# Kernel optimization log

Measured on AMD Instinct MI355X. Metric: run time of the kernel, lower is better.

The kernel has to match this reference:

```python
import jax, jax.numpy as jnp
import numpy as np

B, N = 1, 1024
C_S, C_Z, N_HEAD, C_HEAD = 384, 128, 16, 24
HC = N_HEAD * C_HEAD


def _ln(x, eps=1e-5):
    m = jnp.mean(x, axis=-1, keepdims=True)
    v = jnp.var(x, axis=-1, keepdims=True)
    return (x - m) / jnp.sqrt(v + eps)


def setup_inputs() -> dict:
    key = jax.random.key(0)
    ks = jax.random.split(key, 24)
    w = lambda k, shp: (jax.random.normal(k, shp, jnp.float32) * 0.02)
    return {
        "a_i": jax.random.normal(ks[0], (B, N, C_S), jnp.float32),
        "s_i": jax.random.normal(ks[1], (B, N, C_S), jnp.float32),
        "z_ij": jax.random.normal(ks[2], (B, N, N, C_Z), jnp.float32),
        # AdaLN params
        "adaln_lns_w": jnp.ones((C_S,), jnp.float32),      # layer_norm_s weight (no bias)
        "adaln_ws": w(ks[3], (C_S, C_S)),                   # linear_s weight
        "adaln_bs": jnp.zeros((C_S,), jnp.float32),         # linear_s bias
        "adaln_wns": w(ks[4], (C_S, C_S)),                  # linear_no_bias_s
        # attention projections
        "wq": w(ks[5], (C_S, HC)),
        "bq": jnp.zeros((HC,), jnp.float32),
        "wk": w(ks[6], (C_S, HC)),
        "wv": w(ks[7], (C_S, HC)),
        # pair bias
        "lnb_w": jnp.ones((C_Z,), jnp.float32),
        "lnb_b": jnp.zeros((C_Z,), jnp.float32),
        "wb": w(ks[8], (C_Z, N_HEAD)),
        # gate + output
        "wg": w(ks[9], (C_S, HC)),
        "wo": w(ks[10], (HC, C_S)),
        # final conditioning gate (bias init -2.0 per module)
        "ws": w(ks[11], (C_S, C_S)),
        "bs": jnp.full((C_S,), -2.0, jnp.float32),
    }


def reference(a_i, s_i, z_ij, adaln_lns_w, adaln_ws, adaln_bs, adaln_wns,
              wq, bq, wk, wv, lnb_w, lnb_b, wb, wg, wo, ws, bs):
    b, n, _ = a_i.shape
    H, D = N_HEAD, C_HEAD
    # AdaLN: a <- sigmoid(Lin(s)) * LN(a) + Lin_nb(s)
    a = _ln(a_i)
    s = _ln(s_i) * adaln_lns_w
    a = jax.nn.sigmoid(s @ adaln_ws + adaln_bs) * a + s @ adaln_wns
    # QKV projections -> [b, i, h, d]
    q = (a @ wq + bq).reshape(b, n, H, D)
    k = (a @ wk).reshape(b, n, H, D)
    v = (a @ wv).reshape(b, n, H, D)
    # pair bias [b, h, i, j]
    bias = jnp.einsum('bijc,ch->bhij', _ln(z_ij) * lnb_w + lnb_b, wb)
    # gate [b, i, h, d]
    g = jax.nn.sigmoid(a @ wg).reshape(b, n, H, D)
    logits = jnp.einsum('bihd,bjhd->bhij', q, k) / jnp.sqrt(jnp.float32(D)) + bias
    A = jax.nn.softmax(logits, axis=-1)
    o = jnp.einsum('bhij,bjhd->bihd', A, v) * g
    o = o.reshape(b, n, H * D) @ wo
    # final gate uses raw s_i
    return jax.nn.sigmoid(s_i @ ws + bs) * o
```

## Files before the change

### kernel.cpp

```cpp
#include <hip/hip_runtime.h>
#include <hip/hip_bf16.h>
#include <math.h>

#define N_SEQ 1024
#define CS 384
#define CZ 128
#define NH 16
#define CH 24

typedef float  floatx4 __attribute__((ext_vector_type(4)));
typedef short  shortx8 __attribute__((ext_vector_type(8)));
typedef unsigned int uintx4 __attribute__((ext_vector_type(4)));

__device__ __forceinline__ unsigned short f2bf(float f){
  union { float fv; unsigned u; } c; c.fv = f;
  unsigned u = c.u;
  return (unsigned short)((u + 0x7fffu + ((u >> 16) & 1u)) >> 16);
}
__device__ __forceinline__ float bf2f(unsigned short s){
  union { unsigned u; float fv; } c; c.u = ((unsigned)s) << 16; return c.fv;
}
__device__ __forceinline__ float bf_lo(unsigned u){
  union { unsigned uu; float f; } c; c.uu = u << 16; return c.f;
}
__device__ __forceinline__ float bf_hi(unsigned u){
  union { unsigned uu; float f; } c; c.uu = u & 0xffff0000u; return c.f;
}
__device__ __forceinline__ float sigmoidf_(float x){ return 1.f / (1.f + __expf(-x)); }

__global__ __launch_bounds__(128) void ln_kernel(
    const float* __restrict__ a_i, const float* __restrict__ s_i,
    const float* __restrict__ lns_w,
    float* __restrict__ a_ln, float* __restrict__ s_ln)
{
  int i = blockIdx.x;
  int t = threadIdx.x;
  float av[3], sv[3];
  float sa = 0.f, qa = 0.f, ss = 0.f, qs = 0.f;
  #pragma unroll
  for (int e = 0; e < 3; ++e){
    int c = t + 128*e;
    float a = a_i[(size_t)i*CS + c];
    float s = s_i[(size_t)i*CS + c];
    av[e] = a; sv[e] = s;
    sa += a; qa += a*a; ss += s; qs += s*s;
  }
  #pragma unroll
  for (int off = 1; off < 64; off <<= 1){
    sa += __shfl_xor(sa, off);
    qa += __shfl_xor(qa, off);
    ss += __shfl_xor(ss, off);
    qs += __shfl_xor(qs, off);
  }
  __shared__ float red[2][4];
  if ((t & 63) == 0){
    int w = t >> 6;
    red[w][0] = sa; red[w][1] = qa; red[w][2] = ss; red[w][3] = qs;
  }
  __syncthreads();
  const float inv = 1.f / CS;
  float Sa = red[0][0] + red[1][0];
  float Qa = red[0][1] + red[1][1];
  float Ss = red[0][2] + red[1][2];
  float Qs = red[0][3] + red[1][3];
  float ma = Sa*inv, va = Qa*inv - ma*ma, ra = rsqrtf(va + 1e-5f);
  float ms = Ss*inv, vs = Qs*inv - ms*ms, rs = rsqrtf(vs + 1e-5f);
  #pragma unroll
  for (int e = 0; e < 3; ++e){
    int c = t + 128*e;
    a_ln[(size_t)i*CS + c] = (av[e] - ma) * ra;
    s_ln[(size_t)i*CS + c] = (sv[e] - ms) * rs * lns_w[c];
  }
}

__global__ __launch_bounds__(384) void gemm_kernel(
    const float* __restrict__ X, const float* __restrict__ W1,
    const float* __restrict__ B1, const float* __restrict__ W2,
    const float* __restrict__ extra,
    float* __restrict__ OUT1, float* __restrict__ OUT2, int mode)
{
  int r0 = blockIdx.x * 4;
  int t  = threadIdx.x;
  int ct = t % 96;
  int rg = t / 96;
  int c0 = ct * 4;
  __shared__ float xl[4][CS];
  #pragma unroll
  for (int rr = 0; rr < 4; ++rr)
    xl[rr][t] = X[(size_t)(r0+rr)*CS + t];
  __syncthreads();
  float acc1[4] = {0.f,0.f,0.f,0.f};
  float acc2[4] = {0.f,0.f,0.f,0.f};
  if (mode <= 2){
    for (int k = 0; k < CS; k += 4){
      floatx4 s4 = *(const floatx4*)&xl[rg][k];
      #pragma unroll
      for (int kk = 0; kk < 4; ++kk){
        floatx4 w1 = *(const floatx4*)&W1[(size_t)(k+kk)*CS + c0];
        floatx4 w2 = *(const floatx4*)&W2[(size_t)(k+kk)*CS + c0];
        #pragma unroll
        for (int cc = 0; cc < 4; ++cc){
          acc1[cc] += s4[kk] * w1[cc];
          acc2[cc] += s4[kk] * w2[cc];
        }
      }
    }
  } else {
    for (int k = 0; k < CS; k += 4){
      floatx4 s4 = *(const floatx4*)&xl[rg][k];
      #pragma unroll
      for (int kk = 0; kk < 4; ++kk){
        floatx4 w1 = *(const floatx4*)&W1[(size_t)(k+kk)*CS + c0];
        #pragma unroll
        for (int cc = 0; cc < 4; ++cc)
          acc1[cc] += s4[kk] * w1[cc];
      }
    }
  }
  int r = r0 + rg;
  size_t ob = (size_t)r * CS + c0;
  if (mode == 0){
    #pragma unroll
    for (int cc = 0; cc < 4; ++cc)
      OUT1[ob+cc] = sigmoidf_(acc1[cc] + B1[c0+cc]) * extra[ob+cc] + acc2[cc];
  } else if (mode == 1){
    #pragma unroll
    for (int cc = 0; cc < 4; ++cc){
      OUT1[ob+cc] = acc1[cc] + B1[c0+cc];
      OUT2[ob+cc] = acc2[cc];
    }
  } else if (mode == 2){
    #pragma unroll
    for (int cc = 0; cc < 4; ++cc){
      OUT1[ob+cc] = acc1[cc];
      OUT2[ob+cc] = sigmoidf_(acc2[cc]);
    }
  } else if (mode == 3){
    #pragma unroll
    for (int cc = 0; cc < 4; ++cc)
      OUT1[ob+cc] = acc1[cc];
  } else {
    #pragma unroll
    for (int cc = 0; cc < 4; ++cc)
      OUT1[ob+cc] = sigmoidf_(acc1[cc] + B1[c0+cc]) * extra[ob+cc];
  }
}

__global__ __launch_bounds__(256) void bias_kernel(
    const float* __restrict__ z, const float* __restrict__ lnb_w,
    const float* __restrict__ lnb_b, const float* __restrict__ wb,
    unsigned short* __restrict__ bias)
{
  int i    = blockIdx.x >> 4;
  int j0   = (blockIdx.x & 15) * 64;
  int wave = threadIdx.x >> 6;
  int lane = threadIdx.x & 63;
  int m    = lane & 15;
  int q    = lane >> 4;
  int jbase = j0 + wave * 16;

  shortx8 bfrag[4];
  float sumw = 0.f, sumb = 0.f;
  #pragma unroll
  for (int s = 0; s < 4; ++s){
    #pragma unroll
    for (int jj = 0; jj < 8; ++jj){
      int c = q*8 + jj + 32*s;
      float lw = lnb_w[c];
      float lb = lnb_b[c];
      float w  = wb[c*NH + m];
      bfrag[s][jj] = (short)f2bf(lw * w);
      sumw += lw * w;
      sumb += lb * w;
    }
  }
  sumw += __shfl_xor(sumw, 16); sumw += __shfl_xor(sumw, 32);
  sumb += __shfl_xor(sumb, 16); sumb += __shfl_xor(sumb, 32);

  const float* zrow = z + ((size_t)i * N_SEQ + (size_t)(jbase + m)) * CZ;
  floatx4 acc = {0.f, 0.f, 0.f, 0.f};
  float sum = 0.f, sq = 0.f;
  #pragma unroll
  for (int s = 0; s < 4; ++s){
    floatx4 z0 = *(const floatx4*)(zrow + q*8 + 32*s);
    floatx4 z1 = *(const floatx4*)(zrow + q*8 + 32*s + 4);
    shortx8 af;
    #pragma unroll
    for (int e = 0; e < 4; ++e){
      sum += z0[e]; sq += z0[e]*z0[e];
      sum += z1[e]; sq += z1[e]*z1[e];
      af[e]   = (short)f2bf(z0[e]);
      af[e+4] = (short)f2bf(z1[e]);
    }
    acc = __builtin_amdgcn_mfma_f32_16x16x32_bf16(af, bfrag[s], acc, 0, 0, 0);
  }
  sum += __shfl_xor(sum, 16); sum += __shfl_xor(sum, 32);
  sq  += __shfl_xor(sq , 16); sq  += __shfl_xor(sq , 32);
  float mean = sum * (1.f/CZ);
  float var  = sq  * (1.f/CZ) - mean*mean;
  float rstd = rsqrtf(var + 1e-5f);

  __shared__ float ob[NH][65];
  #pragma unroll
  for (int r = 0; r < 4; ++r){
    int row = q*4 + r;
    float mr = __shfl(mean, row);
    float rr = __shfl(rstd, row);
    ob[m][wave*16 + row] = rr * (acc[r] - mr * sumw) + sumb;
  }
  __syncthreads();
  size_t base = (size_t)i * N_SEQ + j0;
  #pragma unroll
  for (int rep = 0; rep < 4; ++rep){
    int idx = threadIdx.x + rep*256;
    int hh = idx >> 6;
    int jj = idx & 63;
    bias[(size_t)hh * ((size_t)N_SEQ*N_SEQ) + base + jj] = f2bf(ob[hh][jj]);
  }
}

#define TJ 128
#define KROW 20
__global__ __launch_bounds__(256) void attn_kernel(
    const float* __restrict__ qq, const float* __restrict__ kk,
    const float* __restrict__ vv, const float* __restrict__ gg,
    const unsigned short* __restrict__ bias, float* __restrict__ att)
{
  int h  = blockIdx.x & 15;
  int i0 = (blockIdx.x >> 4) * 16;
  int il = threadIdx.x & 15;
  int jg = threadIdx.x >> 4;

  __shared__ unsigned int smem[TJ*KROW*2];

  float qr[24];
  {
    const float* qs = qq + (size_t)(i0+il)*CS + h*CH;
    #pragma unroll
    for (int e = 0; e < 6; ++e){
      floatx4 t4 = *(const floatx4*)(qs + 4*e);
      qr[4*e] = t4[0]; qr[4*e+1] = t4[1]; qr[4*e+2] = t4[2]; qr[4*e+3] = t4[3];
    }
  }
  const float scale = 0.20412414523193154f;
  float lrun = 0.f;
  float o[24];
  #pragma unroll
  for (int d = 0; d < 24; ++d) o[d] = 0.f;

  for (int jt = 0; jt < 8; ++jt){
    __syncthreads();
    {
      int row  = threadIdx.x >> 1;
      int half = threadIdx.x & 1;
      const float* ks = kk + (size_t)(jt*TJ + row)*CS + h*CH + half*12;
      const float* vs = vv + (size_t)(jt*TJ + row)*CS + h*CH + half*12;
      unsigned int* kd = smem + row*KROW + half*6;
      unsigned int* vd = smem + TJ*KROW + row*KROW + half*6;
      #pragma unroll
      for (int e = 0; e < 6; ++e){
        kd[e] = (unsigned)f2bf(ks[2*e]) | ((unsigned)f2bf(ks[2*e+1]) << 16);
        vd[e] = (unsigned)f2bf(vs[2*e]) | ((unsigned)f2bf(vs[2*e+1]) << 16);
      }
    }
    __syncthreads();
    const unsigned short* bptr = bias + (size_t)h*((size_t)N_SEQ*N_SEQ)
                               + (size_t)(i0+il)*N_SEQ + jt*TJ;
    #pragma unroll
    for (int tt = 0; tt < 8; ++tt){
      int jl = jg + 16*tt;
      uintx4 k0 = *(const uintx4*)&smem[jl*KROW];
      uintx4 k1 = *(const uintx4*)&smem[jl*KROW + 4];
      uintx4 k2 = *(const uintx4*)&smem[jl*KROW + 8];
      float dot = 0.f;
      #pragma unroll
      for (int e = 0; e < 4; ++e){
        dot += bf_lo(k0[e])*qr[2*e]      + bf_hi(k0[e])*qr[2*e+1];
        dot += bf_lo(k1[e])*qr[8+2*e]    + bf_hi(k1[e])*qr[8+2*e+1];
        dot += bf_lo(k2[e])*qr[16+2*e]   + bf_hi(k2[e])*qr[16+2*e+1];
      }
      float p = __expf(dot * scale + bf2f(bptr[jl]));
      lrun += p;
      uintx4 v0 = *(const uintx4*)&smem[TJ*KROW + jl*KROW];
      uintx4 v1 = *(const uintx4*)&smem[TJ*KROW + jl*KROW + 4];
      uintx4 v2 = *(const uintx4*)&smem[TJ*KROW + jl*KROW + 8];
      #pragma unroll
      for (int e = 0; e < 4; ++e){
        o[2*e]      += p * bf_lo(v0[e]);  o[2*e+1]    += p * bf_hi(v0[e]);
        o[8+2*e]    += p * bf_lo(v1[e]);  o[8+2*e+1]  += p * bf_hi(v1[e]);
        o[16+2*e]   += p * bf_lo(v2[e]);  o[16+2*e+1] += p * bf_hi(v2[e]);
      }
    }
  }
  __syncthreads();
  #pragma unroll
  for (int d = 0; d < 24; ++d){
    o[d] += __shfl_xor(o[d], 16);
    o[d] += __shfl_xor(o[d], 32);
  }
  lrun += __shfl_xor(lrun, 16);
  lrun += __shfl_xor(lrun, 32);
  float* mgf = (float*)smem;
  int lane = threadIdx.x & 63;
  int w    = threadIdx.x >> 6;
  if (lane < 16){
    float* slot = mgf + (w*16 + lane)*25;
    slot[0] = lrun;
    #pragma unroll
    for (int d = 0; d < 24; ++d) slot[1+d] = o[d];
  }
  __syncthreads();
  if (threadIdx.x < 16){
    int ii = threadIdx.x;
    float L = 0.f, O[24];
    #pragma unroll
    for (int d = 0; d < 24; ++d) O[d] = 0.f;
    for (int w2 = 0; w2 < 4; ++w2){
      const float* slot = mgf + (w2*16 + ii)*25;
      L += slot[0];
      #pragma unroll
      for (int d = 0; d < 24; ++d) O[d] += slot[1+d];
    }
    const float* gs = gg + (size_t)(i0+ii)*CS + h*CH;
    float* os = att + (size_t)(i0+ii)*CS + h*CH;
    float invL = 1.f / L;
    #pragma unroll
    for (int d = 0; d < 24; ++d) os[d] = O[d] * invL * gs[d];
  }
}

extern "C" void kernel_launch(void* const* d_in, const int* in_sizes, int n_in,
                              void* d_out, int out_size, void* d_ws, size_t ws_size,
                              hipStream_t stream) {
  const float* a_i     = (const float*)d_in[0];
  const float* s_i     = (const float*)d_in[1];
  const float* z_ij    = (const float*)d_in[2];
  const float* lns_w   = (const float*)d_in[3];
  const float* ada_ws  = (const float*)d_in[4];
  const float* ada_bs  = (const float*)d_in[5];
  const float* ada_wns = (const float*)d_in[6];
  const float* wq      = (const float*)d_in[7];
  const float* bq      = (const float*)d_in[8];
  const float* wk      = (const float*)d_in[9];
  const float* wv      = (const float*)d_in[10];
  const float* lnb_w   = (const float*)d_in[11];
  const float* lnb_b   = (const float*)d_in[12];
  const float* wb      = (const float*)d_in[13];
  const float* wg      = (const float*)d_in[14];
  const float* wo      = (const float*)d_in[15];
  const float* wsm     = (const float*)d_in[16];
  const float* bsv     = (const float*)d_in[17];

  const size_t RC = (size_t)N_SEQ * CS;
  float* wsf  = (float*)d_ws;
  float* s_ln = wsf;
  float* a_ln = wsf + RC;
  float* a    = wsf + 2*RC;
  float* qv   = wsf + 3*RC;
  float* kv   = wsf + 4*RC;
  float* vvp  = wsf + 5*RC;
  float* gv   = wsf + 6*RC;
  float* attb = wsf + 7*RC;
  float* tmp  = wsf + 8*RC;
  unsigned short* biasw = (unsigned short*)(wsf + 9*RC);

  ln_kernel<<<N_SEQ, 128, 0, stream>>>(a_i, s_i, lns_w, a_ln, s_ln);
  gemm_kernel<<<N_SEQ/4, 384, 0, stream>>>(s_ln, ada_ws, ada_bs, ada_wns, a_ln, a, nullptr, 0);
  gemm_kernel<<<N_SEQ/4, 384, 0, stream>>>(a, wq, bq, wk, nullptr, qv, kv, 1);
  gemm_kernel<<<N_SEQ/4, 384, 0, stream>>>(a, wv, nullptr, wg, nullptr, vvp, gv, 2);
  bias_kernel<<<N_SEQ*16, 256, 0, stream>>>(z_ij, lnb_w, lnb_b, wb, biasw);
  attn_kernel<<<N_SEQ, 256, 0, stream>>>(qv, kv, vvp, gv, biasw, attb);
  gemm_kernel<<<N_SEQ/4, 384, 0, stream>>>(attb, wo, nullptr, nullptr, nullptr, tmp, nullptr, 3);
  gemm_kernel<<<N_SEQ/4, 384, 0, stream>>>(s_i, wsm, bsv, nullptr, tmp, (float*)d_out, nullptr, 4);
}
```

Measured before the change: 1.169 ms.

## Fuse LayerNorm into AdaLN GEMM, merge QKVG and output GEMMs, precompute bias weights

Folds the row LayerNorms into the AdaLN projection kernel and merges the Q/K/V/G projections into one kernel. The two output GEMMs (wo and the s_i gate) become a single kernel, so the intermediate buffers and several launches go away. The folded LayerNorm-times-wb weights and their sums are computed once in a tiny prep kernel rather than in every bias block. The K/V staging in attention now uses vectorized loads and stores. Higher register pressure in the merged GEMM kernels could reduce occupancy.

```diff
diff --git a/kernel.cpp b/kernel.cpp
--- a/kernel.cpp
+++ b/kernel.cpp
@@ -11,6 +11,7 @@
 typedef float  floatx4 __attribute__((ext_vector_type(4)));
 typedef short  shortx8 __attribute__((ext_vector_type(8)));
 typedef unsigned int uintx4 __attribute__((ext_vector_type(4)));
+typedef unsigned int uintx2 __attribute__((ext_vector_type(2)));
 
 __device__ __forceinline__ unsigned short f2bf(float f){
   union { float fv; unsigned u; } c; c.fv = f;
@@ -28,127 +29,213 @@
 }
 __device__ __forceinline__ float sigmoidf_(float x){ return 1.f / (1.f + __expf(-x)); }
 
-__global__ __launch_bounds__(128) void ln_kernel(
+__global__ __launch_bounds__(256) void prep_kernel(
+    const float* __restrict__ lnb_w, const float* __restrict__ lnb_b,
+    const float* __restrict__ wb,
+    unsigned short* __restrict__ wprodT, float* __restrict__ sums)
+{
+  int t = threadIdx.x;
+  int h = t >> 4;
+  int g = t & 15;
+  float pw = 0.f, pb = 0.f;
+  unsigned short loc[8];
+  #pragma unroll
+  for (int e = 0; e < 8; ++e){
+    int c = g*8 + e;
+    float lw = lnb_w[c], lb = lnb_b[c], w = wb[c*NH + h];
+    float p = lw * w;
+    loc[e] = f2bf(p);
+    pw += p; pb += lb * w;
+  }
+  #pragma unroll
+  for (int e = 0; e < 8; ++e) wprodT[h*CZ + g*8 + e] = loc[e];
+  #pragma unroll
+  for (int off = 1; off < 16; off <<= 1){
+    pw += __shfl_xor(pw, off);
+    pb += __shfl_xor(pb, off);
+  }
+  if (g == 0){ sums[h] = pw; sums[16+h] = pb; }
+}
+
+__global__ __launch_bounds__(384) void adaln_kernel(
     const float* __restrict__ a_i, const float* __restrict__ s_i,
     const float* __restrict__ lns_w,
-    float* __restrict__ a_ln, float* __restrict__ s_ln)
-{
-  int i = blockIdx.x;
-  int t = threadIdx.x;
-  float av[3], sv[3];
-  float sa = 0.f, qa = 0.f, ss = 0.f, qs = 0.f;
-  #pragma unroll
-  for (int e = 0; e < 3; ++e){
-    int c = t + 128*e;
-    float a = a_i[(size_t)i*CS + c];
-    float s = s_i[(size_t)i*CS + c];
-    av[e] = a; sv[e] = s;
-    sa += a; qa += a*a; ss += s; qs += s*s;
-  }
-  #pragma unroll
-  for (int off = 1; off < 64; off <<= 1){
-    sa += __shfl_xor(sa, off);
-    qa += __shfl_xor(qa, off);
-    ss += __shfl_xor(ss, off);
-    qs += __shfl_xor(qs, off);
-  }
-  __shared__ float red[2][4];
-  if ((t & 63) == 0){
-    int w = t >> 6;
-    red[w][0] = sa; red[w][1] = qa; red[w][2] = ss; red[w][3] = qs;
-  }
-  __syncthreads();
-  const float inv = 1.f / CS;
-  float Sa = red[0][0] + red[1][0];
-  float Qa = red[0][1] + red[1][1];
-  float Ss = red[0][2] + red[1][2];
-  float Qs = red[0][3] + red[1][3];
-  float ma = Sa*inv, va = Qa*inv - ma*ma, ra = rsqrtf(va + 1e-5f);
-  float ms = Ss*inv, vs = Qs*inv - ms*ms, rs = rsqrtf(vs + 1e-5f);
-  #pragma unroll
-  for (int e = 0; e < 3; ++e){
-    int c = t + 128*e;
-    a_ln[(size_t)i*CS + c] = (av[e] - ma) * ra;
-    s_ln[(size_t)i*CS + c] = (sv[e] - ms) * rs * lns_w[c];
-  }
-}
-
-__global__ __launch_bounds__(384) void gemm_kernel(
-    const float* __restrict__ X, const float* __restrict__ W1,
-    const float* __restrict__ B1, const float* __restrict__ W2,
-    const float* __restrict__ extra,
-    float* __restrict__ OUT1, float* __restrict__ OUT2, int mode)
+    const float* __restrict__ W1, const float* __restrict__ B1,
+    const float* __restrict__ W2, float* __restrict__ OUT)
 {
   int r0 = blockIdx.x * 4;
   int t  = threadIdx.x;
-  int ct = t % 96;
-  int rg = t / 96;
-  int c0 = ct * 4;
-  __shared__ float xl[4][CS];
-  #pragma unroll
-  for (int rr = 0; rr < 4; ++rr)
-    xl[rr][t] = X[(size_t)(r0+rr)*CS + t];
-  __syncthreads();
+  __shared__ float xs[4][CS];
+  __shared__ float xa[4][CS];
+  __shared__ float red[6][16];
+  float av[4], sv[4], pa[4], qa[4], ps[4], qs[4];
+  #pragma unroll
+  for (int rr = 0; rr < 4; ++rr){
+    float a = a_i[(size_t)(r0+rr)*CS + t];
+    float s = s_i[(size_t)(r0+rr)*CS + t];
+    av[rr] = a; sv[rr] = s;
+    pa[rr] = a; qa[rr] = a*a; ps[rr] = s; qs[rr] = s*s;
+  }
+  #pragma unroll
+  for (int off = 1; off < 64; off <<= 1){
+    #pragma unroll
+    for (int rr = 0; rr < 4; ++rr){
+      pa[rr] += __shfl_xor(pa[rr], off);
+      qa[rr] += __shfl_xor(qa[rr], off);
+      ps[rr] += __shfl_xor(ps[rr], off);
+      qs[rr] += __shfl_xor(qs[rr], off);
+    }
+  }
+  int w = t >> 6;
+  if ((t & 63) == 0){
+    #pragma unroll
+    for (int rr = 0; rr < 4; ++rr){
+      red[w][rr] = pa[rr]; red[w][4+rr] = qa[rr];
+      red[w][8+rr] = ps[rr]; red[w][12+rr] = qs[rr];
+    }
+  }
+  __syncthreads();
+  float lw = lns_w[t];
+  const float inv = 1.f / CS;
+  #pragma unroll
+  for (int rr = 0; rr < 4; ++rr){
+    float Sa=0.f, Qa=0.f, Ss=0.f, Qs=0.f;
+    #pragma unroll
+    for (int w2 = 0; w2 < 6; ++w2){
+      Sa += red[w2][rr]; Qa += red[w2][4+rr];
+      Ss += red[w2][8+rr]; Qs += red[w2][12+rr];
+    }
+    float ma = Sa*inv, va = Qa*inv - ma*ma, ra = rsqrtf(va + 1e-5f);
+    float ms = Ss*inv, vs = Qs*inv - ms*ms, rs = rsqrtf(vs + 1e-5f);
+    xa[rr][t] = (av[rr] - ma) * ra;
+    xs[rr][t] = (sv[rr] - ms) * rs * lw;
+  }
+  __syncthreads();
+  int ct = t % 96, rg = t / 96, c0 = ct * 4;
   float acc1[4] = {0.f,0.f,0.f,0.f};
   float acc2[4] = {0.f,0.f,0.f,0.f};
-  if (mode <= 2){
-    for (int k = 0; k < CS; k += 4){
-      floatx4 s4 = *(const floatx4*)&xl[rg][k];
-      #pragma unroll
-      for (int kk = 0; kk < 4; ++kk){
-        floatx4 w1 = *(const floatx4*)&W1[(size_t)(k+kk)*CS + c0];
-        floatx4 w2 = *(const floatx4*)&W2[(size_t)(k+kk)*CS + c0];
-        #pragma unroll
-        for (int cc = 0; cc < 4; ++cc){
-          acc1[cc] += s4[kk] * w1[cc];
-          acc2[cc] += s4[kk] * w2[cc];
-        }
+  #pragma unroll 2
+  for (int k = 0; k < CS; k += 4){
+    floatx4 s4 = *(const floatx4*)&xs[rg][k];
+    floatx4 w1[4], w2[4];
+    #pragma unroll
+    for (int j = 0; j < 4; ++j){
+      size_t o = (size_t)(k+j)*CS + c0;
+      w1[j] = *(const floatx4*)&W1[o];
+      w2[j] = *(const floatx4*)&W2[o];
+    }
+    #pragma unroll
+    for (int j = 0; j < 4; ++j)
+      #pragma unroll
+      for (int cc = 0; cc < 4; ++cc){
+        acc1[cc] += s4[j] * w1[j][cc];
+        acc2[cc] += s4[j] * w2[j][cc];
       }
-    }
-  } else {
-    for (int k = 0; k < CS; k += 4){
-      floatx4 s4 = *(const floatx4*)&xl[rg][k];
-      #pragma unroll
-      for (int kk = 0; kk < 4; ++kk){
-        floatx4 w1 = *(const floatx4*)&W1[(size_t)(k+kk)*CS + c0];
-        #pragma unroll
-        for (int cc = 0; cc < 4; ++cc)
-          acc1[cc] += s4[kk] * w1[cc];
-      }
-    }
   }
   int r = r0 + rg;
   size_t ob = (size_t)r * CS + c0;
-  if (mode == 0){
-    #pragma unroll
-    for (int cc = 0; cc < 4; ++cc)
-      OUT1[ob+cc] = sigmoidf_(acc1[cc] + B1[c0+cc]) * extra[ob+cc] + acc2[cc];
-  } else if (mode == 1){
-    #pragma unroll
-    for (int cc = 0; cc < 4; ++cc){
-      OUT1[ob+cc] = acc1[cc] + B1[c0+cc];
-      OUT2[ob+cc] = acc2[cc];
-    }
-  } else if (mode == 2){
-    #pragma unroll
-    for (int cc = 0; cc < 4; ++cc){
-      OUT1[ob+cc] = acc1[cc];
-      OUT2[ob+cc] = sigmoidf_(acc2[cc]);
-    }
-  } else if (mode == 3){
-    #pragma unroll
-    for (int cc = 0; cc < 4; ++cc)
-      OUT1[ob+cc] = acc1[cc];
-  } else {
-    #pragma unroll
-    for (int cc = 0; cc < 4; ++cc)
-      OUT1[ob+cc] = sigmoidf_(acc1[cc] + B1[c0+cc]) * extra[ob+cc];
-  }
+  #pragma unroll
+  for (int cc = 0; cc < 4; ++cc)
+    OUT[ob+cc] = sigmoidf_(acc1[cc] + B1[c0+cc]) * xa[rg][c0+cc] + acc2[cc];
+}
+
+__global__ __launch_bounds__(384) void qkvg_kernel(
+    const float* __restrict__ A, const float* __restrict__ wq,
+    const float* __restrict__ bq, const float* __restrict__ wk,
+    const float* __restrict__ wv, const float* __restrict__ wg,
+    float* __restrict__ qv, float* __restrict__ kv,
+    float* __restrict__ vv, float* __restrict__ gv)
+{
+  int r0 = blockIdx.x * 4;
+  int t  = threadIdx.x;
+  __shared__ float xl[4][CS];
+  #pragma unroll
+  for (int rr = 0; rr < 4; ++rr)
+    xl[rr][t] = A[(size_t)(r0+rr)*CS + t];
+  __syncthreads();
+  int ct = t % 96, rg = t / 96, c0 = ct * 4;
+  float aq[4]={0.f,0.f,0.f,0.f}, ak[4]={0.f,0.f,0.f,0.f};
+  float av4[4]={0.f,0.f,0.f,0.f}, ag[4]={0.f,0.f,0.f,0.f};
+  #pragma unroll 2
+  for (int k = 0; k < CS; k += 4){
+    floatx4 x4 = *(const floatx4*)&xl[rg][k];
+    floatx4 q[4], kk4[4], v4[4], g4[4];
+    #pragma unroll
+    for (int j = 0; j < 4; ++j){
+      size_t o = (size_t)(k+j)*CS + c0;
+      q[j]   = *(const floatx4*)&wq[o];
+      kk4[j] = *(const floatx4*)&wk[o];
+      v4[j]  = *(const floatx4*)&wv[o];
+      g4[j]  = *(const floatx4*)&wg[o];
+    }
+    #pragma unroll
+    for (int j = 0; j < 4; ++j)
+      #pragma unroll
+      for (int cc = 0; cc < 4; ++cc){
+        aq[cc]  += x4[j] * q[j][cc];
+        ak[cc]  += x4[j] * kk4[j][cc];
+        av4[cc] += x4[j] * v4[j][cc];
+        ag[cc]  += x4[j] * g4[j][cc];
+      }
+  }
+  int r = r0 + rg;
+  size_t ob = (size_t)r * CS + c0;
+  #pragma unroll
+  for (int cc = 0; cc < 4; ++cc){
+    qv[ob+cc] = aq[cc] + bq[c0+cc];
+    kv[ob+cc] = ak[cc];
+    vv[ob+cc] = av4[cc];
+    gv[ob+cc] = sigmoidf_(ag[cc]);
+  }
+}
+
+__global__ __launch_bounds__(384) void final_kernel(
+    const float* __restrict__ att, const float* __restrict__ wo,
+    const float* __restrict__ s_i, const float* __restrict__ wsm,
+    const float* __restrict__ bsv, float* __restrict__ OUT)
+{
+  int r0 = blockIdx.x * 4;
+  int t  = threadIdx.x;
+  __shared__ float xo[4][CS];
+  __shared__ float xsI[4][CS];
+  #pragma unroll
+  for (int rr = 0; rr < 4; ++rr){
+    xo[rr][t]  = att[(size_t)(r0+rr)*CS + t];
+    xsI[rr][t] = s_i[(size_t)(r0+rr)*CS + t];
+  }
+  __syncthreads();
+  int ct = t % 96, rg = t / 96, c0 = ct * 4;
+  float acc1[4] = {0.f,0.f,0.f,0.f};
+  float acc2[4] = {0.f,0.f,0.f,0.f};
+  #pragma unroll 2
+  for (int k = 0; k < CS; k += 4){
+    floatx4 o4 = *(const floatx4*)&xo[rg][k];
+    floatx4 s4 = *(const floatx4*)&xsI[rg][k];
+    floatx4 w1[4], w2[4];
+    #pragma unroll
+    for (int j = 0; j < 4; ++j){
+      size_t o = (size_t)(k+j)*CS + c0;
+      w1[j] = *(const floatx4*)&wo[o];
+      w2[j] = *(const floatx4*)&wsm[o];
+    }
+    #pragma unroll
+    for (int j = 0; j < 4; ++j)
+      #pragma unroll
+      for (int cc = 0; cc < 4; ++cc){
+        acc1[cc] += o4[j] * w1[j][cc];
+        acc2[cc] += s4[j] * w2[j][cc];
+      }
+  }
+  int r = r0 + rg;
+  size_t ob = (size_t)r * CS + c0;
+  #pragma unroll
+  for (int cc = 0; cc < 4; ++cc)
+    OUT[ob+cc] = sigmoidf_(acc2[cc] + bsv[c0+cc]) * acc1[cc];
 }
 
 __global__ __launch_bounds__(256) void bias_kernel(
-    const float* __restrict__ z, const float* __restrict__ lnb_w,
-    const float* __restrict__ lnb_b, const float* __restrict__ wb,
+    const float* __restrict__ z,
+    const unsigned short* __restrict__ wprodT, const float* __restrict__ sums,
     unsigned short* __restrict__ bias)
 {
   int i    = blockIdx.x >> 4;
@@ -159,23 +246,13 @@
   int q    = lane >> 4;
   int jbase = j0 + wave * 16;
 
+  const unsigned short* wp = wprodT + m*CZ;
   shortx8 bfrag[4];
-  float sumw = 0.f, sumb = 0.f;
-  #pragma unroll
-  for (int s = 0; s < 4; ++s){
-    #pragma unroll
-    for (int jj = 0; jj < 8; ++jj){
-      int c = q*8 + jj + 32*s;
-      float lw = lnb_w[c];
-      float lb = lnb_b[c];
-      float w  = wb[c*NH + m];
-      bfrag[s][jj] = (short)f2bf(lw * w);
-      sumw += lw * w;
-      sumb += lb * w;
-    }
-  }
-  sumw += __shfl_xor(sumw, 16); sumw += __shfl_xor(sumw, 32);
-  sumb += __shfl_xor(sumb, 16); sumb += __shfl_xor(sumb, 32);
+  #pragma unroll
+  for (int s = 0; s < 4; ++s)
+    bfrag[s] = *(const shortx8*)(wp + q*8 + 32*s);
+  float sumw = sums[m];
+  float sumb = sums[16+m];
 
   const float* zrow = z + ((size_t)i * N_SEQ + (size_t)(jbase + m)) * CZ;
   floatx4 acc = {0.f, 0.f, 0.f, 0.f};
@@ -255,13 +332,33 @@
       int half = threadIdx.x & 1;
       const float* ks = kk + (size_t)(jt*TJ + row)*CS + h*CH + half*12;
       const float* vs = vv + (size_t)(jt*TJ + row)*CS + h*CH + half*12;
+      floatx4 ka = *(const floatx4*)(ks);
+      floatx4 kb = *(const floatx4*)(ks+4);
+      floatx4 kc = *(const floatx4*)(ks+8);
+      floatx4 va = *(const floatx4*)(vs);
+      floatx4 vb = *(const floatx4*)(vs+4);
+      floatx4 vc = *(const floatx4*)(vs+8);
       unsigned int* kd = smem + row*KROW + half*6;
       unsigned int* vd = smem + TJ*KROW + row*KROW + half*6;
-      #pragma unroll
-      for (int e = 0; e < 6; ++e){
-        kd[e] = (unsigned)f2bf(ks[2*e]) | ((unsigned)f2bf(ks[2*e+1]) << 16);
-        vd[e] = (unsigned)f2bf(vs[2*e]) | ((unsigned)f2bf(vs[2*e+1]) << 16);
-      }
+      uintx2 p0, p1, p2;
+      p0[0] = (unsigned)f2bf(ka[0]) | ((unsigned)f2bf(ka[1])<<16);
+      p0[1] = (unsigned)f2bf(ka[2]) | ((unsigned)f2bf(ka[3])<<16);
+      p1[0] = (unsigned)f2bf(kb[0]) | ((unsigned)f2bf(kb[1])<<16);
+      p1[1] = (unsigned)f2bf(kb[2]) | ((unsigned)f2bf(kb[3])<<16);
+      p2[0] = (unsigned)f2bf(kc[0]) | ((unsigned)f2bf(kc[1])<<16);
+      p2[1] = (unsigned)f2bf(kc[2]) | ((unsigned)f2bf(kc[3])<<16);
+      *(uintx2*)(kd)   = p0;
+      *(uintx2*)(kd+2) = p1;
+      *(uintx2*)(kd+4) = p2;
+      p0[0] = (unsigned)f2bf(va[0]) | ((unsigned)f2bf(va[1])<<16);
+      p0[1] = (unsigned)f2bf(va[2]) | ((unsigned)f2bf(va[3])<<16);
+      p1[0] = (unsigned)f2bf(vb[0]) | ((unsigned)f2bf(vb[1])<<16);
+      p1[1] = (unsigned)f2bf(vb[2]) | ((unsigned)f2bf(vb[3])<<16);
+      p2[0] = (unsigned)f2bf(vc[0]) | ((unsigned)f2bf(vc[1])<<16);
+      p2[1] = (unsigned)f2bf(vc[2]) | ((unsigned)f2bf(vc[3])<<16);
+      *(uintx2*)(vd)   = p0;
+      *(uintx2*)(vd+2) = p1;
+      *(uintx2*)(vd+4) = p2;
     }
     __syncthreads();
     const unsigned short* bptr = bias + (size_t)h*((size_t)N_SEQ*N_SEQ)
@@ -353,23 +450,20 @@
 
   const size_t RC = (size_t)N_SEQ * CS;
   float* wsf  = (float*)d_ws;
-  float* s_ln = wsf;
-  float* a_ln = wsf + RC;
-  float* a    = wsf + 2*RC;
-  float* qv   = wsf + 3*RC;
-  float* kv   = wsf + 4*RC;
-  float* vvp  = wsf + 5*RC;
-  float* gv   = wsf + 6*RC;
-  float* attb = wsf + 7*RC;
-  float* tmp  = wsf + 8*RC;
-  unsigned short* biasw = (unsigned short*)(wsf + 9*RC);
-
-  ln_kernel<<<N_SEQ, 128, 0, stream>>>(a_i, s_i, lns_w, a_ln, s_ln);
-  gemm_kernel<<<N_SEQ/4, 384, 0, stream>>>(s_ln, ada_ws, ada_bs, ada_wns, a_ln, a, nullptr, 0);
-  gemm_kernel<<<N_SEQ/4, 384, 0, stream>>>(a, wq, bq, wk, nullptr, qv, kv, 1);
-  gemm_kernel<<<N_SEQ/4, 384, 0, stream>>>(a, wv, nullptr, wg, nullptr, vvp, gv, 2);
-  bias_kernel<<<N_SEQ*16, 256, 0, stream>>>(z_ij, lnb_w, lnb_b, wb, biasw);
+  float* a    = wsf;
+  float* qv   = wsf + RC;
+  float* kv   = wsf + 2*RC;
+  float* vvp  = wsf + 3*RC;
+  float* gv   = wsf + 4*RC;
+  float* attb = wsf + 5*RC;
+  unsigned short* biasw  = (unsigned short*)(wsf + 6*RC);
+  unsigned short* wprodT = biasw + (size_t)NH*N_SEQ*N_SEQ;
+  float* sums            = (float*)(wprodT + NH*CZ);
+
+  prep_kernel<<<1, 256, 0, stream>>>(lnb_w, lnb_b, wb, wprodT, sums);
+  bias_kernel<<<N_SEQ*16, 256, 0, stream>>>(z_ij, wprodT, sums, biasw);
+  adaln_kernel<<<N_SEQ/4, 384, 0, stream>>>(a_i, s_i, lns_w, ada_ws, ada_bs, ada_wns, a);
+  qkvg_kernel<<<N_SEQ/4, 384, 0, stream>>>(a, wq, bq, wk, wv, wg, qv, kv, vvp, gv);
   attn_kernel<<<N_SEQ, 256, 0, stream>>>(qv, kv, vvp, gv, biasw, attb);
-  gemm_kernel<<<N_SEQ/4, 384, 0, stream>>>(attb, wo, nullptr, nullptr, nullptr, tmp, nullptr, 3);
-  gemm_kernel<<<N_SEQ/4, 384, 0, stream>>>(s_i, wsm, bsv, nullptr, tmp, (float*)d_out, nullptr, 4);
-}
+  final_kernel<<<N_SEQ/4, 384, 0, stream>>>(attb, wo, s_i, wsm, bsv, (float*)d_out);
+}
```

Result: slower. 1.253 ms (+7.2%).
